# Kernel optimization log

Measured on AMD Instinct MI355X. Metric: run time of the kernel, lower is better.

Reference implementation:

```python
import jax, jax.numpy as jnp
import numpy as np

B, C, H, W = 128, 1024, 16, 12
CI = 512              # inter_channels = in_channels // 2
EPS = 1e-4            # module's self.eps for std normalization
BN_EPS = 1e-5         # torch BatchNorm2d default eps (eval mode, running stats)


def setup_inputs() -> dict:
    key = jax.random.key(0)
    ks = jax.random.split(key, 8)
    s_in = 1.0 / np.sqrt(C)
    s_192 = 1.0 / np.sqrt(192)
    s_64 = 1.0 / np.sqrt(64)
    return {
        "x": jax.random.normal(ks[0], (B, C, H, W), jnp.float32),
        "theta_w": jax.random.normal(ks[1], (CI, C), jnp.float32) * s_in,
        "theta_b": jax.random.normal(ks[2], (CI,), jnp.float32) * s_in,
        "phi_w": jax.random.normal(ks[3], (CI, C), jnp.float32) * s_in,
        "phi_b": jax.random.normal(ks[4], (CI,), jnp.float32) * s_in,
        "m1_w": jax.random.normal(ks[5], (64, H * W), jnp.float32) * s_192,
        "m1_b": jax.random.normal(ks[6], (64,), jnp.float32) * s_192,
        "bn_g": jnp.ones((64,), jnp.float32),
        "bn_b": jnp.zeros((64,), jnp.float32),
        "bn_m": jnp.zeros((64,), jnp.float32),
        "bn_v": jnp.ones((64,), jnp.float32),
        "m2_w": jax.random.normal(ks[7], (1, 64), jnp.float32) * s_64,
        "m2_b": jnp.zeros((1,), jnp.float32),
    }


def _conv1x1(x, w, b):
    # x: (B, Cin, H, W), w: (Cout, Cin) -> (B, Cout, H, W)
    return jnp.einsum("bchw,oc->bohw", x, w) + b[None, :, None, None]


def reference(x, theta_w, theta_b, phi_w, phi_b, m1_w, m1_b,
              bn_g, bn_b, bn_m, bn_v, m2_w, m2_b):
    b, c, h, w = x.shape
    hw = h * w

    # theta/phi 1x1 conv projections -> (B, CI, HW)
    theta = _conv1x1(x, theta_w, theta_b).reshape(b, CI, hw)
    phi = _conv1x1(x, phi_w, phi_b).reshape(b, CI, hw)

    # theta_x: (B, HW, CI), z-score over channel axis (torch.std unbiased, ddof=1)
    theta_x = jnp.transpose(theta, (0, 2, 1))
    theta_x = theta_x - jnp.mean(theta_x, axis=2, keepdims=True)
    theta_x = theta_x / (jnp.std(theta_x, axis=2, keepdims=True, ddof=1) + EPS)

    # phi_x: (B, CI, HW), z-score over channel axis (dim 1)
    phi_x = phi - jnp.mean(phi, axis=1, keepdims=True)
    phi_x = phi_x / (jnp.std(phi_x, axis=1, keepdims=True, ddof=1) + EPS)

    # correlation: (B, HW, HW), divided by phi_x.size(1) == CI
    f = jnp.einsum("bnc,bcm->bnm", theta_x, phi_x) / CI

    # transpose then view as (B, HW, H, W) image of correlation maps
    mc = jnp.transpose(f, (0, 2, 1)).reshape(b, hw, h, w)

    # spatial_mask_summary: conv1x1(192->64) -> BN (eval) -> ReLU -> conv1x1(64->1)
    t = _conv1x1(mc, m1_w, m1_b)
    t = (t - bn_m[None, :, None, None]) * (
        bn_g[None, :, None, None] / jnp.sqrt(bn_v + BN_EPS)[None, :, None, None]
    ) + bn_b[None, :, None, None]
    t = jax.nn.relu(t)
    mask = jax.nn.sigmoid(_conv1x1(t, m2_w, m2_b))  # (B, 1, H, W)

    # sigmoid-gated residual
    return x + mask * x
```

## Files before the change

kernel.cpp:

```cpp
#include <hip/hip_runtime.h>

#define B_N 128
#define C_N 1024
#define HW_N 192
#define CI_N 512
#define MROWS (B_N * HW_N)

typedef short bf16x8 __attribute__((ext_vector_type(8)));
typedef float f32x4 __attribute__((ext_vector_type(4)));
typedef unsigned short us4 __attribute__((ext_vector_type(4)));
typedef unsigned short us8 __attribute__((ext_vector_type(8)));

__device__ __forceinline__ unsigned short f2bf(float f){
    unsigned int u = __builtin_bit_cast(unsigned int, f);
    u += 0x7fffu + ((u >> 16) & 1u);
    return (unsigned short)(u >> 16);
}
__device__ __forceinline__ float bf2f(unsigned short h){
    unsigned int u = ((unsigned int)h) << 16;
    return __builtin_bit_cast(float, u);
}
__device__ __forceinline__ void gload_lds16(const void* g, void* l){
    __builtin_amdgcn_global_load_lds(
        (const __attribute__((address_space(1))) unsigned int*)g,
        (__attribute__((address_space(3))) unsigned int*)l, 16, 0, 0);
}

__global__ __launch_bounds__(256) void k_prep_x(const float* __restrict__ x,
                                                unsigned short* __restrict__ xbT){
    __shared__ float tile[64][37];
    int b  = blockIdx.z;
    int c0 = blockIdx.y * 64;
    int n0 = blockIdx.x * 32;
    int t  = threadIdx.x;
    const float* xp = x + (size_t)b * C_N * HW_N;
    int cr = t >> 3;
    int nw = (t & 7) * 4;
    #pragma unroll
    for (int i = 0; i < 2; ++i){
        float4 v = *(const float4*)(xp + (size_t)(c0 + cr + 32 * i) * HW_N + n0 + nw);
        tile[cr + 32 * i][nw + 0] = v.x;
        tile[cr + 32 * i][nw + 1] = v.y;
        tile[cr + 32 * i][nw + 2] = v.z;
        tile[cr + 32 * i][nw + 3] = v.w;
    }
    __syncthreads();
    int nl = t >> 3;
    int j  = t & 7;
    us8 pk;
    #pragma unroll
    for (int e = 0; e < 8; ++e)
        pk[e] = f2bf(tile[j * 8 + e][nl]);
    *(us8*)(xbT + (size_t)(b * HW_N + n0 + nl) * C_N + c0 + j * 8) = pk;
}

__global__ __launch_bounds__(256) void k_prep_w(const float* __restrict__ tw, const float* __restrict__ tb,
                                                const float* __restrict__ pw, const float* __restrict__ pb,
                                                const float* __restrict__ m1w,
                                                unsigned short* __restrict__ Wc, float* __restrict__ bias,
                                                unsigned short* __restrict__ w1b){
    int i = blockIdx.x * 256 + threadIdx.x;
    int o = i >> 10, c = i & 1023;
    float v = (o < 512) ? tw[(size_t)o * 1024 + c] : pw[(size_t)(o - 512) * 1024 + c];
    Wc[i] = f2bf(v);
    if (i < 1024) bias[i] = (i < 512) ? tb[i] : pb[i - 512];
    if (i < 64 * HW_N) w1b[i] = f2bf(m1w[i]);
}

__global__ __launch_bounds__(256, 3) void k_gemm1(const unsigned short* __restrict__ Wc,
                                               const float* __restrict__ bias,
                                               const unsigned short* __restrict__ xbT,
                                               unsigned short* __restrict__ TPt,
                                               float2* __restrict__ part){
    __shared__ __align__(16) unsigned short lW[128 * 64];
    __shared__ __align__(16) unsigned short lX[128 * 64];
    int bid  = blockIdx.x;
    int xcd  = bid & 7;
    int slot = bid >> 3;
    int mb = xcd * 24 + (slot >> 3);
    int nb = slot & 7;
    int tid = threadIdx.x, lane = tid & 63, wave = tid >> 6;
    int wr = wave >> 1, wc = wave & 1;
    int fr = lane & 15, fg = lane >> 4;

    const unsigned short* Wg = Wc  + (size_t)(nb * 128) * C_N;
    const unsigned short* Xg = xbT + (size_t)(mb * 128) * C_N;

    int row0 = tid >> 3;
    int su   = tid & 7;
    int gsw  = (su ^ (row0 & 7)) * 8;
    const unsigned short* wsrc = Wg + (size_t)row0 * C_N + gsw;
    const unsigned short* xsrc = Xg + (size_t)row0 * C_N + gsw;

    f32x4 acc[4][4];
    f32x4 zero = {0.f, 0.f, 0.f, 0.f};
    #pragma unroll
    for (int i = 0; i < 4; ++i)
        #pragma unroll
        for (int j = 0; j < 4; ++j)
            acc[i][j] = zero;

    for (int k0 = 0; k0 < C_N; k0 += 64){
        __syncthreads();
        #pragma unroll
        for (int i = 0; i < 4; ++i){
            gload_lds16(wsrc + (size_t)(32 * i) * C_N + k0, (char*)lW + tid * 16 + i * 4096);
            gload_lds16(xsrc + (size_t)(32 * i) * C_N + k0, (char*)lX + tid * 16 + i * 4096);
        }
        __syncthreads();

        #pragma unroll
        for (int kk = 0; kk < 2; ++kk){
            bf16x8 wf[4], xf[4];
            #pragma unroll
            for (int j = 0; j < 4; ++j){
                int row = wc * 64 + j * 16 + fr;
                int un  = (kk * 4 + fg) ^ (row & 7);
                wf[j] = *(const bf16x8*)((char*)lW + row * 128 + un * 16);
            }
            #pragma unroll
            for (int i = 0; i < 4; ++i){
                int row = wr * 64 + i * 16 + fr;
                int un  = (kk * 4 + fg) ^ (row & 7);
                xf[i] = *(const bf16x8*)((char*)lX + row * 128 + un * 16);
            }
            #pragma unroll
            for (int i = 0; i < 4; ++i)
                #pragma unroll
                for (int j = 0; j < 4; ++j)
                    acc[i][j] = __builtin_amdgcn_mfma_f32_16x16x32_bf16(wf[j], xf[i], acc[i][j], 0, 0, 0);
        }
    }

    float s[4] = {0.f,0.f,0.f,0.f}, q[4] = {0.f,0.f,0.f,0.f};
    #pragma unroll
    for (int i = 0; i < 4; ++i){
        int n = mb * 128 + wr * 64 + i * 16 + fr;
        #pragma unroll
        for (int j = 0; j < 4; ++j){
            int o0 = nb * 128 + wc * 64 + j * 16 + fg * 4;
            float4 b4 = *(const float4*)(bias + o0);
            float v0 = acc[i][j][0] + b4.x;
            float v1 = acc[i][j][1] + b4.y;
            float v2 = acc[i][j][2] + b4.z;
            float v3 = acc[i][j][3] + b4.w;
            s[i] += v0 + v1 + v2 + v3;
            q[i] += v0*v0 + v1*v1 + v2*v2 + v3*v3;
            us4 pk;
            pk[0] = f2bf(v0); pk[1] = f2bf(v1); pk[2] = f2bf(v2); pk[3] = f2bf(v3);
            *(us4*)(TPt + (size_t)n * 1024 + o0) = pk;
        }
    }
    #pragma unroll
    for (int i = 0; i < 4; ++i){
        s[i] += __shfl_xor(s[i], 16); s[i] += __shfl_xor(s[i], 32);
        q[i] += __shfl_xor(q[i], 16); q[i] += __shfl_xor(q[i], 32);
    }
    if (lane < 16){
        int chunk = nb * 2 + wc;
        #pragma unroll
        for (int i = 0; i < 4; ++i){
            int n = mb * 128 + wr * 64 + i * 16 + fr;
            part[(size_t)n * 16 + chunk] = make_float2(s[i], q[i]);
        }
    }
}

__global__ __launch_bounds__(256) void k_stats(const float2* __restrict__ part,
                                               float2* __restrict__ stats){
    int idx = blockIdx.x * 256 + threadIdx.x;
    int n = idx >> 1, h = idx & 1;
    const float2* p = part + (size_t)n * 16 + h * 8;
    float S = 0.f, Q = 0.f;
    #pragma unroll
    for (int k = 0; k < 8; ++k){ float2 v = p[k]; S += v.x; Q += v.y; }
    float mean = S * (1.f / 512.f);
    float var  = (Q - 512.f * mean * mean) * (1.f / 511.f);
    float inv  = 1.f / (sqrtf(fmaxf(var, 0.f)) + 1e-4f);
    stats[idx] = make_float2(mean, inv);
}

__global__ __launch_bounds__(256) void k_gemm2(const unsigned short* __restrict__ TPt,
                                               const float2* __restrict__ stats,
                                               unsigned short* __restrict__ F){
    __shared__ __align__(16) unsigned short lT[64 * 64];
    __shared__ __align__(16) unsigned short lP[64 * 64];
    int b   = blockIdx.z;
    int tn  = blockIdx.y;
    int tm  = blockIdx.x;
    int tid = threadIdx.x, lane = tid & 63, wave = tid >> 6;
    int wr = wave >> 1, wc = wave & 1;
    int fr = lane & 15, fg = lane >> 4;

    int r0 = tid >> 3;
    int su = tid & 7;
    int sw0 = r0 * 128 + ((su ^ (r0 & 7)) * 16);
    int sw1 = (r0 + 32) * 128 + ((su ^ (r0 & 7)) * 16);
    int gn0 = b * HW_N + tn * 64 + r0, gn1 = gn0 + 32;
    int gm0 = b * HW_N + tm * 64 + r0, gm1 = gm0 + 32;
    float2 sT0 = stats[(size_t)gn0 * 2 + 0], sT1 = stats[(size_t)gn1 * 2 + 0];
    float2 sP0 = stats[(size_t)gm0 * 2 + 1], sP1 = stats[(size_t)gm1 * 2 + 1];

    f32x4 acc[2][2];
    f32x4 zero = {0.f, 0.f, 0.f, 0.f};
    #pragma unroll
    for (int i = 0; i < 2; ++i)
        #pragma unroll
        for (int j = 0; j < 2; ++j)
            acc[i][j] = zero;

    for (int k0 = 0; k0 < CI_N; k0 += 64){
        bf16x8 vt0 = *(const bf16x8*)(TPt + (size_t)gn0 * 1024 + k0 + su * 8);
        bf16x8 vt1 = *(const bf16x8*)(TPt + (size_t)gn1 * 1024 + k0 + su * 8);
        bf16x8 vp0 = *(const bf16x8*)(TPt + (size_t)gm0 * 1024 + 512 + k0 + su * 8);
        bf16x8 vp1 = *(const bf16x8*)(TPt + (size_t)gm1 * 1024 + 512 + k0 + su * 8);
        bf16x8 nt0, nt1, np0, np1;
        #pragma unroll
        for (int e = 0; e < 8; ++e){
            nt0[e] = (short)f2bf((bf2f((unsigned short)vt0[e]) - sT0.x) * sT0.y);
            nt1[e] = (short)f2bf((bf2f((unsigned short)vt1[e]) - sT1.x) * sT1.y);
            np0[e] = (short)f2bf((bf2f((unsigned short)vp0[e]) - sP0.x) * sP0.y);
            np1[e] = (short)f2bf((bf2f((unsigned short)vp1[e]) - sP1.x) * sP1.y);
        }
        __syncthreads();
        *(bf16x8*)((char*)lT + sw0) = nt0;
        *(bf16x8*)((char*)lT + sw1) = nt1;
        *(bf16x8*)((char*)lP + sw0) = np0;
        *(bf16x8*)((char*)lP + sw1) = np1;
        __syncthreads();

        #pragma unroll
        for (int kk = 0; kk < 2; ++kk){
            bf16x8 tf[2], pf[2];
            #pragma unroll
            for (int i = 0; i < 2; ++i){
                int row = wr * 32 + i * 16 + fr;
                int un  = (kk * 4 + fg) ^ (row & 7);
                tf[i] = *(const bf16x8*)((char*)lT + row * 128 + un * 16);
            }
            #pragma unroll
            for (int j = 0; j < 2; ++j){
                int row = wc * 32 + j * 16 + fr;
                int un  = (kk * 4 + fg) ^ (row & 7);
                pf[j] = *(const bf16x8*)((char*)lP + row * 128 + un * 16);
            }
            #pragma unroll
            for (int i = 0; i < 2; ++i)
                #pragma unroll
                for (int j = 0; j < 2; ++j)
                    acc[i][j] = __builtin_amdgcn_mfma_f32_16x16x32_bf16(pf[j], tf[i], acc[i][j], 0, 0, 0);
        }
    }

    #pragma unroll
    for (int i = 0; i < 2; ++i){
        int n = tn * 64 + wr * 32 + i * 16 + fr;
        #pragma unroll
        for (int j = 0; j < 2; ++j){
            int m0 = tm * 64 + wc * 32 + j * 16 + fg * 4;
            us4 pk;
            #pragma unroll
            for (int r = 0; r < 4; ++r)
                pk[r] = f2bf(acc[i][j][r] * (1.0f / 512.0f));
            *(us4*)(F + ((size_t)b * HW_N + n) * HW_N + m0) = pk;
        }
    }
}

__global__ __launch_bounds__(256) void k_mask2(const unsigned short* __restrict__ F,
        const unsigned short* __restrict__ w1b, const float* __restrict__ m1b,
        const float* __restrict__ bng, const float* __restrict__ bnb,
        const float* __restrict__ bnm, const float* __restrict__ bnv,
        const float* __restrict__ m2w, const float* __restrict__ m2b,
        float* __restrict__ mask){
    int tid = threadIdx.x, lane = tid & 63, wave = tid >> 6;
    int fr = lane & 15, fg = lane >> 4;
    int row0 = blockIdx.x * 64 + wave * 16;
    const unsigned short* Ag = F + (size_t)row0 * HW_N;

    f32x4 acc[4];
    f32x4 zero = {0.f, 0.f, 0.f, 0.f};
    #pragma unroll
    for (int j = 0; j < 4; ++j) acc[j] = zero;

    #pragma unroll
    for (int kk = 0; kk < 6; ++kk){
        bf16x8 af = *(const bf16x8*)(Ag + (size_t)fr * HW_N + kk * 32 + fg * 8);
        #pragma unroll
        for (int j = 0; j < 4; ++j){
            bf16x8 bfv = *(const bf16x8*)(w1b + (size_t)(j * 16 + fr) * HW_N + kk * 32 + fg * 8);
            acc[j] = __builtin_amdgcn_mfma_f32_16x16x32_bf16(af, bfv, acc[j], 0, 0, 0);
        }
    }

    float sc[4], sh[4], bb[4], w2v[4];
    #pragma unroll
    for (int j = 0; j < 4; ++j){
        int o = j * 16 + fr;
        float s = bng[o] * rsqrtf(bnv[o] + 1e-5f);
        sc[j] = s;
        sh[j] = bnb[o] - bnm[o] * s;
        bb[j] = m1b[o];
        w2v[j] = m2w[o];
    }
    float mb2 = m2b[0];

    #pragma unroll
    for (int r = 0; r < 4; ++r){
        float y = 0.f;
        #pragma unroll
        for (int j = 0; j < 4; ++j){
            float t = fmaxf((acc[j][r] + bb[j]) * sc[j] + sh[j], 0.f);
            y += t * w2v[j];
        }
        y += __shfl_xor(y, 1);
        y += __shfl_xor(y, 2);
        y += __shfl_xor(y, 4);
        y += __shfl_xor(y, 8);
        if (fr == 0)
            mask[row0 + fg * 4 + r] = 1.f / (1.f + __expf(-(y + mb2)));
    }
}

__global__ __launch_bounds__(256) void k_apply(const float* __restrict__ x,
                                               const float* __restrict__ mask,
                                               float* __restrict__ out){
    size_t i4 = (size_t)blockIdx.x * 256 + threadIdx.x;
    size_t e  = i4 * 4;
    float4 v = ((const float4*)x)[i4];
    size_t n = e % HW_N;
    size_t b = e / ((size_t)C_N * HW_N);
    const float* mk = mask + b * HW_N + n;
    float4 o;
    o.x = v.x * (1.f + mk[0]);
    o.y = v.y * (1.f + mk[1]);
    o.z = v.z * (1.f + mk[2]);
    o.w = v.w * (1.f + mk[3]);
    ((float4*)out)[i4] = o;
}

extern "C" void kernel_launch(void* const* d_in, const int* in_sizes, int n_in,
                              void* d_out, int out_size, void* d_ws, size_t ws_size,
                              hipStream_t stream){
    (void)in_sizes; (void)n_in; (void)out_size; (void)ws_size;
    const float* x   = (const float*)d_in[0];
    const float* tw  = (const float*)d_in[1];
    const float* tb  = (const float*)d_in[2];
    const float* pw  = (const float*)d_in[3];
    const float* pb  = (const float*)d_in[4];
    const float* m1w = (const float*)d_in[5];
    const float* m1b = (const float*)d_in[6];
    const float* bng = (const float*)d_in[7];
    const float* bnb = (const float*)d_in[8];
    const float* bnm = (const float*)d_in[9];
    const float* bnv = (const float*)d_in[10];
    const float* m2w = (const float*)d_in[11];
    const float* m2b = (const float*)d_in[12];
    float* out = (float*)d_out;

    char* ws = (char*)d_ws;
    size_t off = 0;
    unsigned short* xbT = (unsigned short*)(ws + off); off += (size_t)MROWS * C_N * 2;
    unsigned short* Wc  = (unsigned short*)(ws + off); off += (size_t)1024 * 1024 * 2;
    float* bias         = (float*)(ws + off);          off += 4096;
    unsigned short* TPt = (unsigned short*)(ws + off); off += (size_t)MROWS * 1024 * 2;
    unsigned short* F   = (unsigned short*)(ws + off); off += (size_t)MROWS * HW_N * 2;
    float* mask         = (float*)(ws + off);          off += (size_t)MROWS * 4;
    unsigned short* w1b = (unsigned short*)(ws + off); off += (size_t)64 * HW_N * 2;
    off = (off + 255) & ~(size_t)255;
    float2* part        = (float2*)(ws + off);         off += (size_t)MROWS * 16 * 8;
    float2* stats       = (float2*)(ws + off);         off += (size_t)MROWS * 2 * 8;

    k_prep_x<<<dim3(6, 16, B_N), 256, 0, stream>>>(x, xbT);
    k_prep_w<<<dim3(4096), 256, 0, stream>>>(tw, tb, pw, pb, m1w, Wc, bias, w1b);
    k_gemm1<<<dim3(1536), 256, 0, stream>>>(Wc, bias, xbT, TPt, part);
    k_stats<<<dim3(MROWS * 2 / 256), 256, 0, stream>>>(part, stats);
    k_gemm2<<<dim3(3, 3, B_N), 256, 0, stream>>>(TPt, stats, F);
    k_mask2<<<dim3(MROWS / 64), 256, 0, stream>>>(F, w1b, m1b, bng, bnb, bnm, bnv, m2w, m2b, mask);
    k_apply<<<dim3(MROWS * C_N / 4 / 256), 256, 0, stream>>>(x, mask, out);
}
```

Measured before the change: 164.8 us.

## Enlarge GEMM1 tiles to 256x256 with double-buffered LDS prefetch

```diff
diff --git a/kernel.cpp b/kernel.cpp
--- a/kernel.cpp
+++ b/kernel.cpp
@@ -67,24 +67,24 @@
     if (i < 64 * HW_N) w1b[i] = f2bf(m1w[i]);
 }
 
-__global__ __launch_bounds__(256, 3) void k_gemm1(const unsigned short* __restrict__ Wc,
+__global__ __launch_bounds__(512, 2) void k_gemm1(const unsigned short* __restrict__ Wc,
                                                const float* __restrict__ bias,
                                                const unsigned short* __restrict__ xbT,
                                                unsigned short* __restrict__ TPt,
                                                float2* __restrict__ part){
-    __shared__ __align__(16) unsigned short lW[128 * 64];
-    __shared__ __align__(16) unsigned short lX[128 * 64];
+    __shared__ __align__(16) unsigned short lW[2][256 * 64];
+    __shared__ __align__(16) unsigned short lX[2][256 * 64];
     int bid  = blockIdx.x;
     int xcd  = bid & 7;
     int slot = bid >> 3;
-    int mb = xcd * 24 + (slot >> 3);
-    int nb = slot & 7;
+    int mb = xcd * 12 + (slot >> 2);
+    int nb = slot & 3;
     int tid = threadIdx.x, lane = tid & 63, wave = tid >> 6;
-    int wr = wave >> 1, wc = wave & 1;
+    int wm = wave >> 2, wn = wave & 3;
     int fr = lane & 15, fg = lane >> 4;
 
-    const unsigned short* Wg = Wc  + (size_t)(nb * 128) * C_N;
-    const unsigned short* Xg = xbT + (size_t)(mb * 128) * C_N;
+    const unsigned short* Wg = Wc  + (size_t)(nb * 256) * C_N;
+    const unsigned short* Xg = xbT + (size_t)(mb * 256) * C_N;
 
     int row0 = tid >> 3;
     int su   = tid & 7;
@@ -92,53 +92,82 @@
     const unsigned short* wsrc = Wg + (size_t)row0 * C_N + gsw;
     const unsigned short* xsrc = Xg + (size_t)row0 * C_N + gsw;
 
-    f32x4 acc[4][4];
+    f32x4 acc[8][4];
     f32x4 zero = {0.f, 0.f, 0.f, 0.f};
     #pragma unroll
-    for (int i = 0; i < 4; ++i)
+    for (int i = 0; i < 8; ++i)
         #pragma unroll
         for (int j = 0; j < 4; ++j)
             acc[i][j] = zero;
 
-    for (int k0 = 0; k0 < C_N; k0 += 64){
-        __syncthreads();
-        #pragma unroll
-        for (int i = 0; i < 4; ++i){
-            gload_lds16(wsrc + (size_t)(32 * i) * C_N + k0, (char*)lW + tid * 16 + i * 4096);
-            gload_lds16(xsrc + (size_t)(32 * i) * C_N + k0, (char*)lX + tid * 16 + i * 4096);
-        }
-        __syncthreads();
-
-        #pragma unroll
-        for (int kk = 0; kk < 2; ++kk){
-            bf16x8 wf[4], xf[4];
-            #pragma unroll
-            for (int j = 0; j < 4; ++j){
-                int row = wc * 64 + j * 16 + fr;
-                int un  = (kk * 4 + fg) ^ (row & 7);
-                wf[j] = *(const bf16x8*)((char*)lW + row * 128 + un * 16);
+    #pragma unroll
+    for (int i = 0; i < 4; ++i){
+        gload_lds16(wsrc + (size_t)(64 * i) * C_N, (char*)lW[0] + tid * 16 + i * 8192);
+        gload_lds16(xsrc + (size_t)(64 * i) * C_N, (char*)lX[0] + tid * 16 + i * 8192);
+    }
+
+    for (int kt = 0; kt < 16; ++kt){
+        int cur = kt & 1;
+        if (kt < 15){
+            int k1 = (kt + 1) * 64;
+            int nxt = cur ^ 1;
+            #pragma unroll
+            for (int i = 0; i < 4; ++i){
+                gload_lds16(wsrc + (size_t)(64 * i) * C_N + k1, (char*)lW[nxt] + tid * 16 + i * 8192);
+                gload_lds16(xsrc + (size_t)(64 * i) * C_N + k1, (char*)lX[nxt] + tid * 16 + i * 8192);
             }
-            #pragma unroll
-            for (int i = 0; i < 4; ++i){
-                int row = wr * 64 + i * 16 + fr;
-                int un  = (kk * 4 + fg) ^ (row & 7);
-                xf[i] = *(const bf16x8*)((char*)lX + row * 128 + un * 16);
+            asm volatile("s_waitcnt vmcnt(8)" ::: "memory");
+        } else {
+            asm volatile("s_waitcnt vmcnt(0)" ::: "memory");
+        }
+        __builtin_amdgcn_s_barrier();
+        __builtin_amdgcn_sched_barrier(0);
+
+        const unsigned short* lw = lW[cur];
+        const unsigned short* lx = lX[cur];
+        bf16x8 vb[4][2];
+        #pragma unroll
+        for (int j = 0; j < 4; ++j){
+            int row = wn * 64 + j * 16 + fr;
+            #pragma unroll
+            for (int kk = 0; kk < 2; ++kk)
+                vb[j][kk] = *(const bf16x8*)((const char*)lw + row * 128 + (((kk * 4 + fg) ^ (row & 7)) * 16));
+        }
+        #pragma unroll
+        for (int q = 0; q < 4; ++q){
+            bf16x8 va[2][2];
+            #pragma unroll
+            for (int di = 0; di < 2; ++di){
+                int row = wm * 128 + (q * 2 + di) * 16 + fr;
+                #pragma unroll
+                for (int kk = 0; kk < 2; ++kk)
+                    va[di][kk] = *(const bf16x8*)((const char*)lx + row * 128 + (((kk * 4 + fg) ^ (row & 7)) * 16));
             }
-            #pragma unroll
-            for (int i = 0; i < 4; ++i)
+            __builtin_amdgcn_s_setprio(1);
+            #pragma unroll
+            for (int kk = 0; kk < 2; ++kk)
                 #pragma unroll
-                for (int j = 0; j < 4; ++j)
-                    acc[i][j] = __builtin_amdgcn_mfma_f32_16x16x32_bf16(wf[j], xf[i], acc[i][j], 0, 0, 0);
-        }
-    }
-
-    float s[4] = {0.f,0.f,0.f,0.f}, q[4] = {0.f,0.f,0.f,0.f};
-    #pragma unroll
-    for (int i = 0; i < 4; ++i){
-        int n = mb * 128 + wr * 64 + i * 16 + fr;
+                for (int di = 0; di < 2; ++di)
+                    #pragma unroll
+                    for (int j = 0; j < 4; ++j)
+                        acc[q * 2 + di][j] = __builtin_amdgcn_mfma_f32_16x16x32_bf16(
+                            vb[j][kk], va[di][kk], acc[q * 2 + di][j], 0, 0, 0);
+            __builtin_amdgcn_s_setprio(0);
+        }
+        asm volatile("s_waitcnt lgkmcnt(0)" ::: "memory");
+        __builtin_amdgcn_sched_barrier(0);
+        __builtin_amdgcn_s_barrier();
+    }
+
+    float s[8], q[8];
+    #pragma unroll
+    for (int i = 0; i < 8; ++i){ s[i] = 0.f; q[i] = 0.f; }
+    #pragma unroll
+    for (int i = 0; i < 8; ++i){
+        int n = mb * 256 + wm * 128 + i * 16 + fr;
         #pragma unroll
         for (int j = 0; j < 4; ++j){
-            int o0 = nb * 128 + wc * 64 + j * 16 + fg * 4;
+            int o0 = nb * 256 + wn * 64 + j * 16 + fg * 4;
             float4 b4 = *(const float4*)(bias + o0);
             float v0 = acc[i][j][0] + b4.x;
             float v1 = acc[i][j][1] + b4.y;
@@ -152,15 +181,15 @@
         }
     }
     #pragma unroll
-    for (int i = 0; i < 4; ++i){
+    for (int i = 0; i < 8; ++i){
         s[i] += __shfl_xor(s[i], 16); s[i] += __shfl_xor(s[i], 32);
         q[i] += __shfl_xor(q[i], 16); q[i] += __shfl_xor(q[i], 32);
     }
-    if (lane < 16){
-        int chunk = nb * 2 + wc;
-        #pragma unroll
-        for (int i = 0; i < 4; ++i){
-            int n = mb * 128 + wr * 64 + i * 16 + fr;
+    if (fg == 0){
+        int chunk = nb * 4 + wn;
+        #pragma unroll
+        for (int i = 0; i < 8; ++i){
+            int n = mb * 256 + wm * 128 + i * 16 + fr;
             part[(size_t)n * 16 + chunk] = make_float2(s[i], q[i]);
         }
     }
@@ -373,7 +402,7 @@
 
     k_prep_x<<<dim3(6, 16, B_N), 256, 0, stream>>>(x, xbT);
     k_prep_w<<<dim3(4096), 256, 0, stream>>>(tw, tb, pw, pb, m1w, Wc, bias, w1b);
-    k_gemm1<<<dim3(1536), 256, 0, stream>>>(Wc, bias, xbT, TPt, part);
+    k_gemm1<<<dim3(384), 512, 0, stream>>>(Wc, bias, xbT, TPt, part);
     k_stats<<<dim3(MROWS * 2 / 256), 256, 0, stream>>>(part, stats);
     k_gemm2<<<dim3(3, 3, B_N), 256, 0, stream>>>(TPt, stats, F);
     k_mask2<<<dim3(MROWS / 64), 256, 0, stream>>>(F, w1b, m1b, bng, bnb, bnm, bnv, m2w, m2b, mask);
```

After: 180.7 us. +9.6%, slower.

## Fuse correlation GEMM with mask MLP, keeping correlation rows in LDS

Applied to the files above, without the earlier changes.

```diff
diff --git a/kernel.cpp b/kernel.cpp
--- a/kernel.cpp
+++ b/kernel.cpp
@@ -180,119 +180,124 @@
     stats[idx] = make_float2(mean, inv);
 }
 
-__global__ __launch_bounds__(256) void k_gemm2(const unsigned short* __restrict__ TPt,
-                                               const float2* __restrict__ stats,
-                                               unsigned short* __restrict__ F){
-    __shared__ __align__(16) unsigned short lT[64 * 64];
-    __shared__ __align__(16) unsigned short lP[64 * 64];
-    int b   = blockIdx.z;
-    int tn  = blockIdx.y;
-    int tm  = blockIdx.x;
-    int tid = threadIdx.x, lane = tid & 63, wave = tid >> 6;
-    int wr = wave >> 1, wc = wave & 1;
-    int fr = lane & 15, fg = lane >> 4;
-
-    int r0 = tid >> 3;
-    int su = tid & 7;
-    int sw0 = r0 * 128 + ((su ^ (r0 & 7)) * 16);
-    int sw1 = (r0 + 32) * 128 + ((su ^ (r0 & 7)) * 16);
-    int gn0 = b * HW_N + tn * 64 + r0, gn1 = gn0 + 32;
-    int gm0 = b * HW_N + tm * 64 + r0, gm1 = gm0 + 32;
-    float2 sT0 = stats[(size_t)gn0 * 2 + 0], sT1 = stats[(size_t)gn1 * 2 + 0];
-    float2 sP0 = stats[(size_t)gm0 * 2 + 1], sP1 = stats[(size_t)gm1 * 2 + 1];
-
-    f32x4 acc[2][2];
-    f32x4 zero = {0.f, 0.f, 0.f, 0.f};
-    #pragma unroll
-    for (int i = 0; i < 2; ++i)
-        #pragma unroll
-        for (int j = 0; j < 2; ++j)
-            acc[i][j] = zero;
-
-    for (int k0 = 0; k0 < CI_N; k0 += 64){
-        bf16x8 vt0 = *(const bf16x8*)(TPt + (size_t)gn0 * 1024 + k0 + su * 8);
-        bf16x8 vt1 = *(const bf16x8*)(TPt + (size_t)gn1 * 1024 + k0 + su * 8);
-        bf16x8 vp0 = *(const bf16x8*)(TPt + (size_t)gm0 * 1024 + 512 + k0 + su * 8);
-        bf16x8 vp1 = *(const bf16x8*)(TPt + (size_t)gm1 * 1024 + 512 + k0 + su * 8);
-        bf16x8 nt0, nt1, np0, np1;
-        #pragma unroll
-        for (int e = 0; e < 8; ++e){
-            nt0[e] = (short)f2bf((bf2f((unsigned short)vt0[e]) - sT0.x) * sT0.y);
-            nt1[e] = (short)f2bf((bf2f((unsigned short)vt1[e]) - sT1.x) * sT1.y);
-            np0[e] = (short)f2bf((bf2f((unsigned short)vp0[e]) - sP0.x) * sP0.y);
-            np1[e] = (short)f2bf((bf2f((unsigned short)vp1[e]) - sP1.x) * sP1.y);
-        }
-        __syncthreads();
-        *(bf16x8*)((char*)lT + sw0) = nt0;
-        *(bf16x8*)((char*)lT + sw1) = nt1;
-        *(bf16x8*)((char*)lP + sw0) = np0;
-        *(bf16x8*)((char*)lP + sw1) = np1;
-        __syncthreads();
-
-        #pragma unroll
-        for (int kk = 0; kk < 2; ++kk){
-            bf16x8 tf[2], pf[2];
-            #pragma unroll
-            for (int i = 0; i < 2; ++i){
-                int row = wr * 32 + i * 16 + fr;
-                int un  = (kk * 4 + fg) ^ (row & 7);
-                tf[i] = *(const bf16x8*)((char*)lT + row * 128 + un * 16);
-            }
-            #pragma unroll
-            for (int j = 0; j < 2; ++j){
-                int row = wc * 32 + j * 16 + fr;
-                int un  = (kk * 4 + fg) ^ (row & 7);
-                pf[j] = *(const bf16x8*)((char*)lP + row * 128 + un * 16);
-            }
-            #pragma unroll
-            for (int i = 0; i < 2; ++i)
-                #pragma unroll
-                for (int j = 0; j < 2; ++j)
-                    acc[i][j] = __builtin_amdgcn_mfma_f32_16x16x32_bf16(pf[j], tf[i], acc[i][j], 0, 0, 0);
-        }
-    }
-
-    #pragma unroll
-    for (int i = 0; i < 2; ++i){
-        int n = tn * 64 + wr * 32 + i * 16 + fr;
-        #pragma unroll
-        for (int j = 0; j < 2; ++j){
-            int m0 = tm * 64 + wc * 32 + j * 16 + fg * 4;
-            us4 pk;
-            #pragma unroll
-            for (int r = 0; r < 4; ++r)
-                pk[r] = f2bf(acc[i][j][r] * (1.0f / 512.0f));
-            *(us4*)(F + ((size_t)b * HW_N + n) * HW_N + m0) = pk;
-        }
-    }
-}
-
-__global__ __launch_bounds__(256) void k_mask2(const unsigned short* __restrict__ F,
+__global__ __launch_bounds__(256) void k_gemm2m(const unsigned short* __restrict__ TPt,
+        const float2* __restrict__ stats,
         const unsigned short* __restrict__ w1b, const float* __restrict__ m1b,
         const float* __restrict__ bng, const float* __restrict__ bnb,
         const float* __restrict__ bnm, const float* __restrict__ bnv,
         const float* __restrict__ m2w, const float* __restrict__ m2b,
         float* __restrict__ mask){
+    __shared__ __align__(16) unsigned short lT[64 * 64];
+    __shared__ __align__(16) unsigned short lP[192 * 64];
+    __shared__ __align__(16) unsigned short lF[64 * 200];
+    int tn = blockIdx.x;
+    int b  = blockIdx.y;
     int tid = threadIdx.x, lane = tid & 63, wave = tid >> 6;
+    int wr = wave >> 1, wc = wave & 1;
     int fr = lane & 15, fg = lane >> 4;
-    int row0 = blockIdx.x * 64 + wave * 16;
-    const unsigned short* Ag = F + (size_t)row0 * HW_N;
-
-    f32x4 acc[4];
+
+    int rbase = tid >> 3;
+    int su    = tid & 7;
+    const unsigned short* src[8];
+    float2 st[8];
+    unsigned short* dst[8];
+    #pragma unroll
+    for (int i = 0; i < 8; ++i){
+        int srow = rbase + 32 * i;
+        int swz  = (su ^ (srow & 7)) * 16;
+        if (i < 2){
+            int gn = b * HW_N + tn * 64 + srow;
+            src[i] = TPt + (size_t)gn * 1024 + su * 8;
+            st[i]  = stats[(size_t)gn * 2 + 0];
+            dst[i] = (unsigned short*)((char*)lT + srow * 128 + swz);
+        } else {
+            int prow = srow - 64;
+            int gm = b * HW_N + prow;
+            src[i] = TPt + (size_t)gm * 1024 + 512 + su * 8;
+            st[i]  = stats[(size_t)gm * 2 + 1];
+            dst[i] = (unsigned short*)((char*)lP + prow * 128 + swz);
+        }
+    }
+
+    f32x4 acc[3][2][2];
     f32x4 zero = {0.f, 0.f, 0.f, 0.f};
     #pragma unroll
-    for (int j = 0; j < 4; ++j) acc[j] = zero;
-
+    for (int t = 0; t < 3; ++t)
+        #pragma unroll
+        for (int i = 0; i < 2; ++i)
+            #pragma unroll
+            for (int j = 0; j < 2; ++j)
+                acc[t][i][j] = zero;
+
+    for (int k0 = 0; k0 < CI_N; k0 += 64){
+        bf16x8 nv[8];
+        #pragma unroll
+        for (int i = 0; i < 8; ++i){
+            bf16x8 v = *(const bf16x8*)(src[i] + k0);
+            #pragma unroll
+            for (int e = 0; e < 8; ++e)
+                nv[i][e] = (short)f2bf((bf2f((unsigned short)v[e]) - st[i].x) * st[i].y);
+        }
+        __syncthreads();
+        #pragma unroll
+        for (int i = 0; i < 8; ++i)
+            *(bf16x8*)dst[i] = nv[i];
+        __syncthreads();
+
+        #pragma unroll
+        for (int kk = 0; kk < 2; ++kk){
+            bf16x8 tf[2];
+            #pragma unroll
+            for (int i = 0; i < 2; ++i){
+                int row = wr * 32 + i * 16 + fr;
+                int un  = (kk * 4 + fg) ^ (row & 7);
+                tf[i] = *(const bf16x8*)((char*)lT + row * 128 + un * 16);
+            }
+            #pragma unroll
+            for (int t = 0; t < 3; ++t){
+                #pragma unroll
+                for (int j = 0; j < 2; ++j){
+                    int row = t * 64 + wc * 32 + j * 16 + fr;
+                    int un  = (kk * 4 + fg) ^ (row & 7);
+                    bf16x8 pf = *(const bf16x8*)((char*)lP + row * 128 + un * 16);
+                    #pragma unroll
+                    for (int i = 0; i < 2; ++i)
+                        acc[t][i][j] = __builtin_amdgcn_mfma_f32_16x16x32_bf16(pf, tf[i], acc[t][i][j], 0, 0, 0);
+                }
+            }
+        }
+    }
+
+    __syncthreads();
+    #pragma unroll
+    for (int t = 0; t < 3; ++t)
+        #pragma unroll
+        for (int i = 0; i < 2; ++i){
+            int n = wr * 32 + i * 16 + fr;
+            #pragma unroll
+            for (int j = 0; j < 2; ++j){
+                int m0 = t * 64 + wc * 32 + j * 16 + fg * 4;
+                us4 pk;
+                #pragma unroll
+                for (int r = 0; r < 4; ++r)
+                    pk[r] = f2bf(acc[t][i][j][r] * (1.0f / 512.0f));
+                *(us4*)((char*)lF + ((size_t)n * 200 + m0) * 2) = pk;
+            }
+        }
+    __syncthreads();
+
+    f32x4 macc[4];
+    #pragma unroll
+    for (int j = 0; j < 4; ++j) macc[j] = zero;
     #pragma unroll
     for (int kk = 0; kk < 6; ++kk){
-        bf16x8 af = *(const bf16x8*)(Ag + (size_t)fr * HW_N + kk * 32 + fg * 8);
+        bf16x8 af = *(const bf16x8*)((char*)lF + ((size_t)(wave * 16 + fr) * 200 + kk * 32 + fg * 8) * 2);
         #pragma unroll
         for (int j = 0; j < 4; ++j){
             bf16x8 bfv = *(const bf16x8*)(w1b + (size_t)(j * 16 + fr) * HW_N + kk * 32 + fg * 8);
-            acc[j] = __builtin_amdgcn_mfma_f32_16x16x32_bf16(af, bfv, acc[j], 0, 0, 0);
-        }
-    }
-
+            macc[j] = __builtin_amdgcn_mfma_f32_16x16x32_bf16(af, bfv, macc[j], 0, 0, 0);
+        }
+    }
     float sc[4], sh[4], bb[4], w2v[4];
     #pragma unroll
     for (int j = 0; j < 4; ++j){
@@ -304,13 +309,12 @@
         w2v[j] = m2w[o];
     }
     float mb2 = m2b[0];
-
     #pragma unroll
     for (int r = 0; r < 4; ++r){
         float y = 0.f;
         #pragma unroll
         for (int j = 0; j < 4; ++j){
-            float t = fmaxf((acc[j][r] + bb[j]) * sc[j] + sh[j], 0.f);
+            float t = fmaxf((macc[j][r] + bb[j]) * sc[j] + sh[j], 0.f);
             y += t * w2v[j];
         }
         y += __shfl_xor(y, 1);
@@ -318,7 +322,7 @@
         y += __shfl_xor(y, 4);
         y += __shfl_xor(y, 8);
         if (fr == 0)
-            mask[row0 + fg * 4 + r] = 1.f / (1.f + __expf(-(y + mb2)));
+            mask[(size_t)b * HW_N + tn * 64 + wave * 16 + fg * 4 + r] = 1.f / (1.f + __expf(-(y + mb2)));
     }
 }
 
@@ -364,7 +368,6 @@
     unsigned short* Wc  = (unsigned short*)(ws + off); off += (size_t)1024 * 1024 * 2;
     float* bias         = (float*)(ws + off);          off += 4096;
     unsigned short* TPt = (unsigned short*)(ws + off); off += (size_t)MROWS * 1024 * 2;
-    unsigned short* F   = (unsigned short*)(ws + off); off += (size_t)MROWS * HW_N * 2;
     float* mask         = (float*)(ws + off);          off += (size_t)MROWS * 4;
     unsigned short* w1b = (unsigned short*)(ws + off); off += (size_t)64 * HW_N * 2;
     off = (off + 255) & ~(size_t)255;
@@ -375,7 +378,6 @@
     k_prep_w<<<dim3(4096), 256, 0, stream>>>(tw, tb, pw, pb, m1w, Wc, bias, w1b);
     k_gemm1<<<dim3(1536), 256, 0, stream>>>(Wc, bias, xbT, TPt, part);
     k_stats<<<dim3(MROWS * 2 / 256), 256, 0, stream>>>(part, stats);
-    k_gemm2<<<dim3(3, 3, B_N), 256, 0, stream>>>(TPt, stats, F);
-    k_mask2<<<dim3(MROWS / 64), 256, 0, stream>>>(F, w1b, m1b, bng, bnb, bnm, bnv, m2w, m2b, mask);
+    k_gemm2m<<<dim3(3, B_N), 256, 0, stream>>>(TPt, stats, w1b, m1b, bng, bnb, bnm, bnv, m2w, m2b, mask);
     k_apply<<<dim3(MROWS * C_N / 4 / 256), 256, 0, stream>>>(x, mask, out);
 }
```

Result: no change. 164.7 us (-0.1%).
